# Kernel optimization log

Hardware: AMD Instinct MI355X
Metric: run time of the kernel (lower is better)

Reference implementation:

```python
import jax, jax.numpy as jnp
import numpy as np

N_NODES = 100000
N_EDGES = 1600000
D_IN = 50
HIDDEN = 128
N_CLASSES = 8


def setup_inputs() -> dict:
    key = jax.random.key(0)
    ks = jax.random.split(key, 8)
    x = jax.random.normal(ks[0], (N_NODES, D_IN), dtype=jnp.float32)
    edge_index = jax.random.randint(ks[1], (2, N_EDGES), 0, N_NODES, dtype=jnp.int64)
    s1 = 1.0 / np.sqrt(D_IN)
    s2 = 1.0 / np.sqrt(HIDDEN)
    return {
        "x": x,
        "edge_index": edge_index,
        "W1_l": jax.random.normal(ks[2], (D_IN, HIDDEN), dtype=jnp.float32) * s1,
        "W1_r": jax.random.normal(ks[3], (D_IN, HIDDEN), dtype=jnp.float32) * s1,
        "b1": jnp.zeros((HIDDEN,), dtype=jnp.float32),
        "W2_l": jax.random.normal(ks[4], (HIDDEN, N_CLASSES), dtype=jnp.float32) * s2,
        "W2_r": jax.random.normal(ks[5], (HIDDEN, N_CLASSES), dtype=jnp.float32) * s2,
        "b2": jnp.zeros((N_CLASSES,), dtype=jnp.float32),
    }


def _sage_conv(h, src, dst, n_nodes, W_l, W_r, b):
    # mean aggregation of neighbor messages src -> dst
    msg = h[src]                                                   # [E, d]
    agg = jax.ops.segment_sum(msg, dst, num_segments=n_nodes)      # [N, d]
    deg = jax.ops.segment_sum(jnp.ones((src.shape[0], 1), h.dtype), dst,
                              num_segments=n_nodes)                # [N, 1]
    agg = agg / jnp.maximum(deg, 1.0)
    # PyG SAGEConv: lin_l(aggregated) + lin_r(root), bias in lin_l
    return agg @ W_l + h @ W_r + b


def reference(x, edge_index, W1_l, W1_r, b1, W2_l, W2_r, b2):
    n_nodes = x.shape[0]
    src, dst = edge_index[0], edge_index[1]
    h = jax.nn.relu(_sage_conv(x, src, dst, n_nodes, W1_l, W1_r, b1))
    # dropout p=0.5 is identity in eval mode (deterministic baseline)
    return _sage_conv(h, src, dst, n_nodes, W2_l, W2_r, b2)
```

## Files before the change

### kernel.cpp

```cpp
#include <hip/hip_runtime.h>

#define N_NODES 100000
#define N_EDGES 1600000
#define D_IN    50
#define HIDDEN  128
#define NCLS    8

#define TILE    2048
#define NTILES  ((N_EDGES + TILE - 1) / TILE)
#define BSHIFT  9
#define NB      196

#define PREP_CONVX_BLOCKS 12500
#define PREP_W_BLOCKS     36

#define LW 68

typedef __bf16 bf16_t;
typedef bf16_t bf16x8 __attribute__((ext_vector_type(8)));
typedef float  f32x4  __attribute__((ext_vector_type(4)));

__device__ __forceinline__ unsigned f2bf(float f) {
    union { float f; unsigned u; } a; a.f = f;
    unsigned u = a.u;
    return (u + 0x7FFFu + ((u >> 16) & 1u)) >> 16;
}
__device__ __forceinline__ unsigned pack2(float a, float b) {
    return f2bf(a) | (f2bf(b) << 16);
}
__device__ __forceinline__ float bf_lo(unsigned v) { return __uint_as_float(v << 16); }
__device__ __forceinline__ float bf_hi(unsigned v) { return __uint_as_float(v & 0xFFFF0000u); }

#define ACC4(a, u) { a[0]+=bf_lo(u.x); a[1]+=bf_hi(u.x); a[2]+=bf_lo(u.y); a[3]+=bf_hi(u.y); \
                     a[4]+=bf_lo(u.z); a[5]+=bf_hi(u.z); a[6]+=bf_lo(u.w); a[7]+=bf_hi(u.w); }

__global__ __launch_bounds__(256) void prep_kernel(
    const float* __restrict__ x,
    const int*   __restrict__ dst,
    const float* __restrict__ W1l, const float* __restrict__ W1r,
    const float* __restrict__ W2l, const float* __restrict__ W2r,
    unsigned* __restrict__ xb, unsigned* __restrict__ acat,
    int* __restrict__ g_hist,
    unsigned* __restrict__ Wt1g, unsigned* __restrict__ W2tg)
{
    __shared__ int lh[NB];
    int blk = blockIdx.x;
    int tid = threadIdx.x;

    if (blk < PREP_CONVX_BLOCKS) {
        int t = blk * 256 + tid;
        int n = t >> 5, j = t & 31;
        if (j < 25) {
            float2 v = ((const float2*)x)[n * 25 + j];
            unsigned pk = pack2(v.x, v.y);
            xb[n * 32 + j] = pk;
            acat[(size_t)n * 64 + 25 + j] = pk;
        } else {
            xb[n * 32 + j] = 0u;
            int z = n * 64 + 50 + (j - 25) * 2;
            acat[z] = 0u;
            acat[z + 1] = 0u;
        }
    } else if (blk < PREP_CONVX_BLOCKS + NTILES) {
        int tile = blk - PREP_CONVX_BLOCKS;
        for (int i = tid; i < NB; i += 256) lh[i] = 0;
        __syncthreads();
        int base = tile * TILE;
        int cnt = min(TILE, N_EDGES - base);
        for (int i = tid; i < cnt; i += 256)
            atomicAdd(&lh[dst[base + i] >> BSHIFT], 1);
        __syncthreads();
        for (int i = tid; i < NB; i += 256)
            g_hist[tile * NB + i] = lh[i];
    } else {
        int t = (blk - PREP_CONVX_BLOCKS - NTILES) * 256 + tid;
        if (t < 8192) {
            int n = t >> 6, kp = t & 63;
            int k0 = kp * 2, k1 = k0 + 1;
            float v0 = (k0 < 50) ? W1l[k0 * 128 + n] : ((k0 < 100) ? W1r[(k0 - 50) * 128 + n] : 0.0f);
            float v1 = (k1 < 50) ? W1l[k1 * 128 + n] : ((k1 < 100) ? W1r[(k1 - 50) * 128 + n] : 0.0f);
            Wt1g[t] = pack2(v0, v1);
        } else if (t < 8192 + 1024) {
            int u = t - 8192;
            int n2 = u >> 6, kp = u & 63;
            int k0 = kp * 2;
            float v0 = (n2 < 8) ? W2l[k0 * 8 + n2] : W2r[k0 * 8 + n2 - 8];
            float v1 = (n2 < 8) ? W2l[(k0 + 1) * 8 + n2] : W2r[(k0 + 1) * 8 + n2 - 8];
            W2tg[u] = pack2(v0, v1);
        }
    }
}

__global__ __launch_bounds__(512) void passB_kernel(
    int* __restrict__ g_hist, int* __restrict__ btot)
{
    __shared__ int s[512];
    int b = blockIdx.x, tid = threadIdx.x;
    int t0 = 2 * tid, t1 = 2 * tid + 1;
    int v0 = (t0 < NTILES) ? g_hist[t0 * NB + b] : 0;
    int v1 = (t1 < NTILES) ? g_hist[t1 * NB + b] : 0;
    int v = v0 + v1;
    s[tid] = v;
    __syncthreads();
    for (int d = 1; d < 512; d <<= 1) {
        int t = (tid >= d) ? s[tid - d] : 0;
        __syncthreads();
        s[tid] += t;
        __syncthreads();
    }
    int ex = s[tid] - v;
    if (t0 < NTILES) g_hist[t0 * NB + b] = ex;
    if (t1 < NTILES) g_hist[t1 * NB + b] = ex + v0;
    if (tid == 511) btot[b] = s[511];
}

__global__ __launch_bounds__(256) void passB2_kernel(
    const int* __restrict__ btot, int* __restrict__ bbase, int* __restrict__ offs)
{
    __shared__ int s[256];
    int tid = threadIdx.x;
    int v = (tid < NB) ? btot[tid] : 0;
    s[tid] = v;
    __syncthreads();
    for (int d = 1; d < 256; d <<= 1) {
        int t = (tid >= d) ? s[tid - d] : 0;
        __syncthreads();
        s[tid] += t;
        __syncthreads();
    }
    if (tid < NB) bbase[tid] = s[tid] - v;
    if (tid == 0) offs[N_NODES] = N_EDGES;
}

__global__ __launch_bounds__(256) void passC_kernel(
    const int* __restrict__ src, const int* __restrict__ dst,
    const int* __restrict__ g_hist, const int* __restrict__ bbase,
    unsigned* __restrict__ bk_pack)
{
    __shared__ int hist[NB];
    __shared__ int seg[NB];
    __shared__ int cur[NB];
    __shared__ int gof[NB];
    __shared__ int sc[256];
    __shared__ unsigned s_pack[TILE];
    __shared__ unsigned short s_bkt[TILE];

    int tid = threadIdx.x, tile = blockIdx.x;
    int base = tile * TILE;
    int cnt = min(TILE, N_EDGES - base);

    for (int i = tid; i < NB; i += 256) {
        hist[i] = 0;
        gof[i] = g_hist[tile * NB + i] + bbase[i];
    }
    __syncthreads();

    int es[8], ed[8];
    #pragma unroll
    for (int k = 0; k < 8; ++k) {
        int i = tid + k * 256;
        if (i < cnt) {
            es[k] = src[base + i];
            ed[k] = dst[base + i];
            atomicAdd(&hist[ed[k] >> BSHIFT], 1);
        }
    }
    __syncthreads();

    {
        int v = (tid < NB) ? hist[tid] : 0;
        sc[tid] = v;
        __syncthreads();
        for (int d = 1; d < 256; d <<= 1) {
            int t = (tid >= d) ? sc[tid - d] : 0;
            __syncthreads();
            sc[tid] += t;
            __syncthreads();
        }
        if (tid < NB) { seg[tid] = sc[tid] - v; cur[tid] = sc[tid] - v; }
    }
    __syncthreads();

    #pragma unroll
    for (int k = 0; k < 8; ++k) {
        int i = tid + k * 256;
        if (i < cnt) {
            int b = ed[k] >> BSHIFT;
            int p = atomicAdd(&cur[b], 1);
            s_pack[p] = (unsigned)es[k] | ((unsigned)(ed[k] & 511) << 17);
            s_bkt[p] = (unsigned short)b;
        }
    }
    __syncthreads();

    for (int i = tid; i < cnt; i += 256) {
        int b = s_bkt[i];
        int g = gof[b] + (i - seg[b]);
        bk_pack[g] = s_pack[i];
    }
}

__global__ __launch_bounds__(512) void passD_kernel(
    const unsigned* __restrict__ bk_pack,
    const int* __restrict__ bbase, const int* __restrict__ btot,
    int* __restrict__ sorted_src, int* __restrict__ offs)
{
    __shared__ int ldeg[512];
    __shared__ int lofs[512];
    int b = blockIdx.x, tid = threadIdx.x;
    int ebase = bbase[b];
    int ecnt = btot[b];
    int nbase = b << BSHIFT;

    ldeg[tid] = 0;
    __syncthreads();
    for (int i = tid; i < ecnt; i += 512)
        atomicAdd(&ldeg[bk_pack[ebase + i] >> 17], 1);
    __syncthreads();

    int v = ldeg[tid];
    lofs[tid] = v;
    __syncthreads();
    for (int d = 1; d < 512; d <<= 1) {
        int t = (tid >= d) ? lofs[tid - d] : 0;
        __syncthreads();
        lofs[tid] += t;
        __syncthreads();
    }
    int ex = lofs[tid] - v;

    int node = nbase + tid;
    if (node < N_NODES) offs[node] = ebase + ex;

    ldeg[tid] = ex;
    __syncthreads();
    for (int i = tid; i < ecnt; i += 512) {
        unsigned pk = bk_pack[ebase + i];
        int p = atomicAdd(&ldeg[pk >> 17], 1);
        sorted_src[ebase + p] = (int)(pk & 0x1FFFFu);
    }
}

__global__ __launch_bounds__(256) void agg_x_kernel(
    const uint4* __restrict__ xb4,
    const int*   __restrict__ offs,
    const int*   __restrict__ ss,
    unsigned* __restrict__ acat)
{
    int node = blockIdx.x * 4 + (threadIdx.x >> 6);
    int lane = threadIdx.x & 63;
    int slot = lane >> 3;
    int ld   = lane & 7;
    if (node >= N_NODES) return;
    int beg = offs[node], end = offs[node + 1];
    float a0[8] = {0,0,0,0,0,0,0,0};
    float a1[8] = {0,0,0,0,0,0,0,0};
    int i = beg;
    for (; i + 15 < end; i += 16) {
        int s0 = ss[i + slot];
        int s1 = ss[i + slot + 8];
        uint4 u0 = xb4[s0 * 8 + ld];
        uint4 u1 = xb4[s1 * 8 + ld];
        ACC4(a0, u0);
        ACC4(a1, u1);
    }
    for (; i + 7 < end; i += 8) {
        uint4 u = xb4[ss[i + slot] * 8 + ld];
        ACC4(a0, u);
    }
    int rem = end - i;
    if (slot < rem) {
        uint4 u = xb4[ss[i + slot] * 8 + ld];
        ACC4(a1, u);
    }
    float t[8];
    #pragma unroll
    for (int k = 0; k < 8; ++k) {
        float v = a0[k] + a1[k];
        v += __shfl_xor(v, 8);
        v += __shfl_xor(v, 16);
        v += __shfl_xor(v, 32);
        t[k] = v;
    }
    if (slot == 0) {
        float inv = 1.0f / fmaxf((float)(end - beg), 1.0f);
        if (ld < 6) {
            uint4 o;
            o.x = pack2(t[0] * inv, t[1] * inv);
            o.y = pack2(t[2] * inv, t[3] * inv);
            o.z = pack2(t[4] * inv, t[5] * inv);
            o.w = pack2(t[6] * inv, t[7] * inv);
            *((uint4*)(acat + (size_t)node * 64 + ld * 4)) = o;
        } else if (ld == 6) {
            acat[(size_t)node * 64 + 24] = pack2(t[0] * inv, t[1] * inv);
        }
    }
}

__global__ __launch_bounds__(256) void fused_mlp_kernel(
    const unsigned* __restrict__ Acat,
    const unsigned* __restrict__ Wt1g,
    const unsigned* __restrict__ W2tg,
    const float* __restrict__ b1,
    const float* __restrict__ b2,
    unsigned* __restrict__ pb,
    float* __restrict__ q)
{
    __shared__ unsigned sWt[128 * LW];
    __shared__ unsigned sW2t[16 * LW];
    __shared__ bf16_t   sH[4][16 * 136];

    int tid = threadIdx.x;
    for (int t = tid; t < 128 * 64; t += 256)
        sWt[(t >> 6) * LW + (t & 63)] = Wt1g[t];
    for (int t = tid; t < 16 * 64; t += 256)
        sW2t[(t >> 6) * LW + (t & 63)] = W2tg[t];
    __syncthreads();

    const int w    = tid >> 6;
    const int lane = tid & 63;
    const int lo   = lane & 15;
    const int g    = lane >> 4;

    float b1v[8][4];
    #pragma unroll
    for (int nt = 0; nt < 8; ++nt)
        #pragma unroll
        for (int r = 0; r < 4; ++r)
            b1v[nt][r] = b1[nt * 16 + g * 4 + r];
    float b2v[4];
    #pragma unroll
    for (int r = 0; r < 4; ++r)
        b2v[r] = (g >= 2) ? b2[(g - 2) * 4 + r] : 0.0f;

    bf16_t* myH = &sH[w][0];

    for (int tile = blockIdx.x; tile * 64 < N_NODES; tile += gridDim.x) {
        int node = tile * 64 + w * 16 + lo;
        int nclamp = min(node, N_NODES - 1);

        int4 bi[4];
        #pragma unroll
        for (int ks = 0; ks < 4; ++ks)
            bi[ks] = *((const int4*)(Acat + (size_t)nclamp * 64 + ks * 16 + g * 4));

        f32x4 acc[8];
        #pragma unroll
        for (int nt = 0; nt < 8; ++nt) acc[nt] = (f32x4)0.0f;
        #pragma unroll
        for (int nt = 0; nt < 8; ++nt) {
            #pragma unroll
            for (int ks = 0; ks < 4; ++ks) {
                int4 ai = *((const int4*)(sWt + (nt * 16 + lo) * LW + ks * 16 + g * 4));
                acc[nt] = __builtin_amdgcn_mfma_f32_16x16x32_bf16(
                    __builtin_bit_cast(bf16x8, ai),
                    __builtin_bit_cast(bf16x8, bi[ks]), acc[nt], 0, 0, 0);
            }
        }

        #pragma unroll
        for (int nt = 0; nt < 8; ++nt) {
            union { bf16_t h[4]; uint2 u; } pk;
            #pragma unroll
            for (int r = 0; r < 4; ++r)
                pk.h[r] = (bf16_t)fmaxf(acc[nt][r] + b1v[nt][r], 0.0f);
            *((uint2*)(myH + lo * 136 + nt * 16 + g * 4)) = pk.u;
        }
        __syncthreads();

        f32x4 acc2 = (f32x4)0.0f;
        #pragma unroll
        for (int ks = 0; ks < 4; ++ks) {
            int4 a2 = *((const int4*)(sW2t + lo * LW + ks * 16 + g * 4));
            int4 h2 = *((const int4*)(myH + lo * 136 + ks * 32 + g * 8));
            acc2 = __builtin_amdgcn_mfma_f32_16x16x32_bf16(
                __builtin_bit_cast(bf16x8, a2),
                __builtin_bit_cast(bf16x8, h2), acc2, 0, 0, 0);
        }

        if (node < N_NODES) {
            if (g < 2) {
                union { bf16_t h[4]; uint2 u; } pk;
                #pragma unroll
                for (int r = 0; r < 4; ++r) pk.h[r] = (bf16_t)acc2[r];
                *((uint2*)(pb + (size_t)node * 4 + g * 2)) = pk.u;
            } else {
                float4 qq;
                qq.x = acc2[0] + b2v[0];
                qq.y = acc2[1] + b2v[1];
                qq.z = acc2[2] + b2v[2];
                qq.w = acc2[3] + b2v[3];
                *((float4*)(q + (size_t)node * 8 + (g - 2) * 4)) = qq;
            }
        }
        __syncthreads();
    }
}

__global__ __launch_bounds__(256) void aggp_final_kernel(
    const unsigned* __restrict__ pb,
    const float*    __restrict__ q,
    const int*      __restrict__ offs,
    const int*      __restrict__ ss,
    float* __restrict__ out)
{
    int node = blockIdx.x * 4 + (threadIdx.x >> 6);
    int lane = threadIdx.x & 63;
    int k  = lane >> 2;
    int c2 = lane & 3;
    if (node >= N_NODES) return;
    int beg = offs[node], end = offs[node + 1];
    float2 acc = make_float2(0.0f, 0.0f);
    int i = beg + k;
    int sNext = (i < end) ? ss[i] : 0;
    for (; i < end; i += 16) {
        int s = sNext;
        int i2 = i + 16;
        sNext = (i2 < end) ? ss[i2] : 0;
        unsigned v = pb[s * 4 + c2];
        acc.x += bf_lo(v);
        acc.y += bf_hi(v);
    }
    acc.x += __shfl_xor(acc.x, 4);  acc.y += __shfl_xor(acc.y, 4);
    acc.x += __shfl_xor(acc.x, 8);  acc.y += __shfl_xor(acc.y, 8);
    acc.x += __shfl_xor(acc.x, 16); acc.y += __shfl_xor(acc.y, 16);
    acc.x += __shfl_xor(acc.x, 32); acc.y += __shfl_xor(acc.y, 32);
    if (lane < 4) {
        float inv = 1.0f / fmaxf((float)(end - beg), 1.0f);
        float2 qq = ((const float2*)(q + (size_t)node * NCLS))[c2];
        ((float2*)(out + (size_t)node * NCLS))[c2] =
            make_float2(acc.x * inv + qq.x, acc.y * inv + qq.y);
    }
}

extern "C" void kernel_launch(void* const* d_in, const int* in_sizes, int n_in,
                              void* d_out, int out_size, void* d_ws, size_t ws_size,
                              hipStream_t stream)
{
    const float* x   = (const float*)d_in[0];
    const int*   ei  = (const int*)  d_in[1];
    const float* W1l = (const float*)d_in[2];
    const float* W1r = (const float*)d_in[3];
    const float* b1  = (const float*)d_in[4];
    const float* W2l = (const float*)d_in[5];
    const float* W2r = (const float*)d_in[6];
    const float* b2  = (const float*)d_in[7];
    float* out = (float*)d_out;

    const int* src = ei;
    const int* dst = ei + N_EDGES;

    int* ws = (int*)d_ws;
    int*      offs       = ws;
    int*      g_hist     = offs + (N_NODES + 4);
    int*      btot       = g_hist + (NTILES * NB + 4);
    int*      bbase      = btot + 512;
    int*      sorted_src = bbase + 512;
    unsigned* xb         = (unsigned*)(sorted_src + N_EDGES);
    unsigned* Acat       = xb + (size_t)N_NODES * 32;
    unsigned* Wt1g       = Acat + (size_t)N_NODES * 64;
    unsigned* W2tg       = Wt1g + 8192;
    unsigned* pb         = W2tg + 1024;
    float*    q          = (float*)(pb + (size_t)N_NODES * 4);
    unsigned* bk_pack    = (unsigned*)(q + (size_t)N_NODES * 8);

    prep_kernel<<<PREP_CONVX_BLOCKS + NTILES + PREP_W_BLOCKS, 256, 0, stream>>>(
        x, dst, W1l, W1r, W2l, W2r, xb, Acat, g_hist, Wt1g, W2tg);

    passB_kernel <<<NB, 512, 0, stream>>>(g_hist, btot);
    passB2_kernel<<<1, 256, 0, stream>>>(btot, bbase, offs);
    passC_kernel <<<NTILES, 256, 0, stream>>>(src, dst, g_hist, bbase, bk_pack);
    passD_kernel <<<NB, 512, 0, stream>>>(bk_pack, bbase, btot, sorted_src, offs);

    agg_x_kernel<<<(N_NODES + 3) / 4, 256, 0, stream>>>(
        (const uint4*)xb, offs, sorted_src, Acat);

    fused_mlp_kernel<<<512, 256, 0, stream>>>(Acat, Wt1g, W2tg, b1, b2, pb, q);

    aggp_final_kernel<<<(N_NODES + 3) / 4, 256, 0, stream>>>(
        (const unsigned*)pb, q, offs, sorted_src, out);
}
```

Baseline: 127.1 us.

## Fuse counting-sort passes into one cooperative kernel with grid syncs

Replaces the histogram, per-bucket scan, bucket-base scan, scatter and per-node sort kernels with a single cooperative kernel of NTILES (782) blocks separated by grid.sync calls. The histogram moves out of prep_kernel into the cooperative kernel, and the bucket-base scan is recomputed redundantly in each block instead of running as a separate single-block kernel. The aim is to remove several kernel launch gaps. In exchange it relies on all 782 blocks being co-resident, adds grid-wide barrier cost, and the launch return value is ignored, so a failed launch would go unnoticed.

Result: slower. 370.8 us (+191.7%).

```diff
diff --git a/kernel.cpp b/kernel.cpp
--- a/kernel.cpp
+++ b/kernel.cpp
@@ -1,4 +1,7 @@
 #include <hip/hip_runtime.h>
+#include <hip/hip_cooperative_groups.h>
+
+namespace cg = cooperative_groups;
 
 #define N_NODES 100000
 #define N_EDGES 1600000
@@ -36,14 +39,11 @@
 
 __global__ __launch_bounds__(256) void prep_kernel(
     const float* __restrict__ x,
-    const int*   __restrict__ dst,
     const float* __restrict__ W1l, const float* __restrict__ W1r,
     const float* __restrict__ W2l, const float* __restrict__ W2r,
     unsigned* __restrict__ xb, unsigned* __restrict__ acat,
-    int* __restrict__ g_hist,
     unsigned* __restrict__ Wt1g, unsigned* __restrict__ W2tg)
 {
-    __shared__ int lh[NB];
     int blk = blockIdx.x;
     int tid = threadIdx.x;
 
@@ -61,19 +61,8 @@
             acat[z] = 0u;
             acat[z + 1] = 0u;
         }
-    } else if (blk < PREP_CONVX_BLOCKS + NTILES) {
-        int tile = blk - PREP_CONVX_BLOCKS;
-        for (int i = tid; i < NB; i += 256) lh[i] = 0;
-        __syncthreads();
-        int base = tile * TILE;
-        int cnt = min(TILE, N_EDGES - base);
-        for (int i = tid; i < cnt; i += 256)
-            atomicAdd(&lh[dst[base + i] >> BSHIFT], 1);
-        __syncthreads();
-        for (int i = tid; i < NB; i += 256)
-            g_hist[tile * NB + i] = lh[i];
     } else {
-        int t = (blk - PREP_CONVX_BLOCKS - NTILES) * 256 + tid;
+        int t = (blk - PREP_CONVX_BLOCKS) * 256 + tid;
         if (t < 8192) {
             int n = t >> 6, kp = t & 63;
             int k0 = kp * 2, k1 = k0 + 1;
@@ -91,83 +80,97 @@
     }
 }
 
-__global__ __launch_bounds__(512) void passB_kernel(
-    int* __restrict__ g_hist, int* __restrict__ btot)
+__global__ __launch_bounds__(256) void sort_coop_kernel(
+    const int* __restrict__ src, const int* __restrict__ dst,
+    int* __restrict__ g_hist, int* __restrict__ btot,
+    unsigned* __restrict__ bk_pack,
+    int* __restrict__ sorted_src, int* __restrict__ offs)
 {
-    __shared__ int s[512];
-    int b = blockIdx.x, tid = threadIdx.x;
-    int t0 = 2 * tid, t1 = 2 * tid + 1;
-    int v0 = (t0 < NTILES) ? g_hist[t0 * NB + b] : 0;
-    int v1 = (t1 < NTILES) ? g_hist[t1 * NB + b] : 0;
-    int v = v0 + v1;
-    s[tid] = v;
-    __syncthreads();
-    for (int d = 1; d < 512; d <<= 1) {
-        int t = (tid >= d) ? s[tid - d] : 0;
-        __syncthreads();
-        s[tid] += t;
-        __syncthreads();
-    }
-    int ex = s[tid] - v;
-    if (t0 < NTILES) g_hist[t0 * NB + b] = ex;
-    if (t1 < NTILES) g_hist[t1 * NB + b] = ex + v0;
-    if (tid == 511) btot[b] = s[511];
-}
-
-__global__ __launch_bounds__(256) void passB2_kernel(
-    const int* __restrict__ btot, int* __restrict__ bbase, int* __restrict__ offs)
-{
-    __shared__ int s[256];
-    int tid = threadIdx.x;
-    int v = (tid < NB) ? btot[tid] : 0;
-    s[tid] = v;
-    __syncthreads();
-    for (int d = 1; d < 256; d <<= 1) {
-        int t = (tid >= d) ? s[tid - d] : 0;
-        __syncthreads();
-        s[tid] += t;
-        __syncthreads();
-    }
-    if (tid < NB) bbase[tid] = s[tid] - v;
-    if (tid == 0) offs[N_NODES] = N_EDGES;
-}
-
-__global__ __launch_bounds__(256) void passC_kernel(
-    const int* __restrict__ src, const int* __restrict__ dst,
-    const int* __restrict__ g_hist, const int* __restrict__ bbase,
-    unsigned* __restrict__ bk_pack)
-{
-    __shared__ int hist[NB];
-    __shared__ int seg[NB];
-    __shared__ int cur[NB];
-    __shared__ int gof[NB];
-    __shared__ int sc[256];
-    __shared__ unsigned s_pack[TILE];
-    __shared__ unsigned short s_bkt[TILE];
-
-    int tid = threadIdx.x, tile = blockIdx.x;
-    int base = tile * TILE;
-    int cnt = min(TILE, N_EDGES - base);
-
-    for (int i = tid; i < NB; i += 256) {
-        hist[i] = 0;
-        gof[i] = g_hist[tile * NB + i] + bbase[i];
-    }
-    __syncthreads();
-
-    int es[8], ed[8];
-    #pragma unroll
-    for (int k = 0; k < 8; ++k) {
-        int i = tid + k * 256;
-        if (i < cnt) {
-            es[k] = src[base + i];
-            ed[k] = dst[base + i];
-            atomicAdd(&hist[ed[k] >> BSHIFT], 1);
-        }
-    }
-    __syncthreads();
+    cg::grid_group grid = cg::this_grid();
+    __shared__ int sm[4112];
+    const int blk = blockIdx.x;
+    const int tid = threadIdx.x;
 
     {
+        int* lh = sm;
+        for (int i = tid; i < NB; i += 256) lh[i] = 0;
+        __syncthreads();
+        int base = blk * TILE;
+        int cnt = min(TILE, N_EDGES - base);
+        for (int i = tid; i < cnt; i += 256)
+            atomicAdd(&lh[dst[base + i] >> BSHIFT], 1);
+        __syncthreads();
+        for (int i = tid; i < NB; i += 256) g_hist[blk * NB + i] = lh[i];
+    }
+    grid.sync();
+
+    if (blk < NB) {
+        int* s = sm;
+        int b = blk;
+        int t4 = tid * 4;
+        int vloc[4]; int sum = 0;
+        #pragma unroll
+        for (int k = 0; k < 4; ++k) {
+            int t = t4 + k;
+            vloc[k] = (t < NTILES) ? g_hist[t * NB + b] : 0;
+            sum += vloc[k];
+        }
+        s[tid] = sum;
+        __syncthreads();
+        for (int d = 1; d < 256; d <<= 1) {
+            int t = (tid >= d) ? s[tid - d] : 0;
+            __syncthreads();
+            s[tid] += t;
+            __syncthreads();
+        }
+        int ex = s[tid] - sum;
+        #pragma unroll
+        for (int k = 0; k < 4; ++k) {
+            int t = t4 + k;
+            if (t < NTILES) g_hist[t * NB + b] = ex;
+            ex += vloc[k];
+        }
+        if (tid == 255) btot[b] = s[255];
+    }
+    grid.sync();
+
+    {
+        int* hist = sm;
+        int* seg  = sm + 196;
+        int* cur  = sm + 392;
+        int* gof  = sm + 588;
+        int* sc   = sm + 784;
+        unsigned* s_pack = (unsigned*)(sm + 1040);
+        unsigned short* s_bkt = (unsigned short*)(sm + 3088);
+
+        int vb = (tid < NB) ? btot[tid] : 0;
+        sc[tid] = vb;
+        __syncthreads();
+        for (int d = 1; d < 256; d <<= 1) {
+            int t = (tid >= d) ? sc[tid - d] : 0;
+            __syncthreads();
+            sc[tid] += t;
+            __syncthreads();
+        }
+        int bbase_t = sc[tid] - vb;
+        if (tid < NB) gof[tid] = g_hist[blk * NB + tid] + bbase_t;
+        for (int i = tid; i < NB; i += 256) hist[i] = 0;
+        __syncthreads();
+
+        int base = blk * TILE;
+        int cnt = min(TILE, N_EDGES - base);
+        int es[8], ed[8];
+        #pragma unroll
+        for (int k = 0; k < 8; ++k) {
+            int i = tid + k * 256;
+            if (i < cnt) {
+                es[k] = src[base + i];
+                ed[k] = dst[base + i];
+                atomicAdd(&hist[ed[k] >> BSHIFT], 1);
+            }
+        }
+        __syncthreads();
+
         int v = (tid < NB) ? hist[tid] : 0;
         sc[tid] = v;
         __syncthreads();
@@ -178,66 +181,82 @@
             __syncthreads();
         }
         if (tid < NB) { seg[tid] = sc[tid] - v; cur[tid] = sc[tid] - v; }
-    }
-    __syncthreads();
-
-    #pragma unroll
-    for (int k = 0; k < 8; ++k) {
-        int i = tid + k * 256;
-        if (i < cnt) {
-            int b = ed[k] >> BSHIFT;
-            int p = atomicAdd(&cur[b], 1);
-            s_pack[p] = (unsigned)es[k] | ((unsigned)(ed[k] & 511) << 17);
-            s_bkt[p] = (unsigned short)b;
-        }
-    }
-    __syncthreads();
-
-    for (int i = tid; i < cnt; i += 256) {
-        int b = s_bkt[i];
-        int g = gof[b] + (i - seg[b]);
-        bk_pack[g] = s_pack[i];
-    }
-}
-
-__global__ __launch_bounds__(512) void passD_kernel(
-    const unsigned* __restrict__ bk_pack,
-    const int* __restrict__ bbase, const int* __restrict__ btot,
-    int* __restrict__ sorted_src, int* __restrict__ offs)
-{
-    __shared__ int ldeg[512];
-    __shared__ int lofs[512];
-    int b = blockIdx.x, tid = threadIdx.x;
-    int ebase = bbase[b];
-    int ecnt = btot[b];
-    int nbase = b << BSHIFT;
-
-    ldeg[tid] = 0;
-    __syncthreads();
-    for (int i = tid; i < ecnt; i += 512)
-        atomicAdd(&ldeg[bk_pack[ebase + i] >> 17], 1);
-    __syncthreads();
-
-    int v = ldeg[tid];
-    lofs[tid] = v;
-    __syncthreads();
-    for (int d = 1; d < 512; d <<= 1) {
-        int t = (tid >= d) ? lofs[tid - d] : 0;
-        __syncthreads();
-        lofs[tid] += t;
-        __syncthreads();
-    }
-    int ex = lofs[tid] - v;
-
-    int node = nbase + tid;
-    if (node < N_NODES) offs[node] = ebase + ex;
-
-    ldeg[tid] = ex;
-    __syncthreads();
-    for (int i = tid; i < ecnt; i += 512) {
-        unsigned pk = bk_pack[ebase + i];
-        int p = atomicAdd(&ldeg[pk >> 17], 1);
-        sorted_src[ebase + p] = (int)(pk & 0x1FFFFu);
+        __syncthreads();
+
+        #pragma unroll
+        for (int k = 0; k < 8; ++k) {
+            int i = tid + k * 256;
+            if (i < cnt) {
+                int b = ed[k] >> BSHIFT;
+                int p = atomicAdd(&cur[b], 1);
+                s_pack[p] = (unsigned)es[k] | ((unsigned)(ed[k] & 511) << 17);
+                s_bkt[p] = (unsigned short)b;
+            }
+        }
+        __syncthreads();
+
+        for (int i = tid; i < cnt; i += 256) {
+            int b = s_bkt[i];
+            int g = gof[b] + (i - seg[b]);
+            bk_pack[g] = s_pack[i];
+        }
+    }
+    grid.sync();
+
+    if (blk < NB) {
+        int* ldeg = sm;
+        int* s    = sm + 512;
+        int* shr  = sm + 768;
+        int b = blk;
+
+        int vb = (tid < NB) ? btot[tid] : 0;
+        s[tid] = vb;
+        __syncthreads();
+        for (int d = 1; d < 256; d <<= 1) {
+            int t = (tid >= d) ? s[tid - d] : 0;
+            __syncthreads();
+            s[tid] += t;
+            __syncthreads();
+        }
+        if (tid == b) shr[0] = s[tid] - vb;
+        __syncthreads();
+        int ebase = shr[0];
+        int ecnt = btot[b];
+        int nbase = b << BSHIFT;
+
+        ldeg[tid] = 0;
+        ldeg[tid + 256] = 0;
+        __syncthreads();
+        for (int i = tid; i < ecnt; i += 256)
+            atomicAdd(&ldeg[bk_pack[ebase + i] >> 17], 1);
+        __syncthreads();
+
+        int v0 = ldeg[2 * tid], v1 = ldeg[2 * tid + 1];
+        int pv = v0 + v1;
+        s[tid] = pv;
+        __syncthreads();
+        for (int d = 1; d < 256; d <<= 1) {
+            int t = (tid >= d) ? s[tid - d] : 0;
+            __syncthreads();
+            s[tid] += t;
+            __syncthreads();
+        }
+        int ex = s[tid] - pv;
+
+        int n0 = nbase + 2 * tid;
+        if (n0 < N_NODES)     offs[n0]     = ebase + ex;
+        if (n0 + 1 < N_NODES) offs[n0 + 1] = ebase + ex + v0;
+        __syncthreads();
+        ldeg[2 * tid]     = ex;
+        ldeg[2 * tid + 1] = ex + v0;
+        __syncthreads();
+
+        for (int i = tid; i < ecnt; i += 256) {
+            unsigned pk = bk_pack[ebase + i];
+            int p = atomicAdd(&ldeg[pk >> 17], 1);
+            sorted_src[ebase + p] = (int)(pk & 0x1FFFFu);
+        }
+        if (b == 0 && tid == 0) offs[N_NODES] = N_EDGES;
     }
 }
 
@@ -464,13 +483,17 @@
     float*    q          = (float*)(pb + (size_t)N_NODES * 4);
     unsigned* bk_pack    = (unsigned*)(q + (size_t)N_NODES * 8);
 
-    prep_kernel<<<PREP_CONVX_BLOCKS + NTILES + PREP_W_BLOCKS, 256, 0, stream>>>(
-        x, dst, W1l, W1r, W2l, W2r, xb, Acat, g_hist, Wt1g, W2tg);
-
-    passB_kernel <<<NB, 512, 0, stream>>>(g_hist, btot);
-    passB2_kernel<<<1, 256, 0, stream>>>(btot, bbase, offs);
-    passC_kernel <<<NTILES, 256, 0, stream>>>(src, dst, g_hist, bbase, bk_pack);
-    passD_kernel <<<NB, 512, 0, stream>>>(bk_pack, bbase, btot, sorted_src, offs);
+    prep_kernel<<<PREP_CONVX_BLOCKS + PREP_W_BLOCKS, 256, 0, stream>>>(
+        x, W1l, W1r, W2l, W2r, xb, Acat, Wt1g, W2tg);
+
+    {
+        void* args[] = {
+            (void*)&src, (void*)&dst, (void*)&g_hist, (void*)&btot,
+            (void*)&bk_pack, (void*)&sorted_src, (void*)&offs
+        };
+        (void)hipLaunchCooperativeKernel((const void*)sort_coop_kernel,
+                                         dim3(NTILES), dim3(256), args, 0, stream);
+    }
 
     agg_x_kernel<<<(N_NODES + 3) / 4, 256, 0, stream>>>(
         (const uint4*)xb, offs, sorted_src, Acat);
```
